# Kernel tuning notes

Hardware: AMD Instinct MI355X
Metric: run time of the kernel (lower is better)

Reference implementation:

```python
import jax, jax.numpy as jnp
import numpy as np

N, M, D, S = 4, 256, 32, 32


def setup_inputs() -> dict:
    key = jax.random.key(0)
    k1, k2 = jax.random.split(key)
    inputs = jax.random.normal(k1, (N, M, M, D), dtype=jnp.float32)
    mask = jnp.ones((N, M, 1), dtype=bool)
    coeffs = jax.random.normal(k2, (D, S, 15), dtype=jnp.float32) * np.sqrt(2.0) / (D + S)
    diag_bias = jnp.zeros((1, S, 1, 1), dtype=jnp.float32)
    all_bias = jnp.zeros((1, S, 1, 1), dtype=jnp.float32)
    return {"inputs": inputs, "mask": mask, "coeffs": coeffs,
            "diag_bias": diag_bias, "all_bias": all_bias}


def _contractions_2_to_2(x):
    # x: [N, D, m, m]; returns list of 15 [N, D, m, m] basis tensors ('inf' normalization)
    n, d, m, _ = x.shape
    diag = jnp.diagonal(x, axis1=2, axis2=3)            # [N, D, m]
    sum_diag = jnp.sum(diag, axis=2, keepdims=True)      # [N, D, 1]
    rows = jnp.sum(x, axis=3)                            # [N, D, m]
    cols = jnp.sum(x, axis=2)                            # [N, D, m]
    tot = jnp.sum(rows, axis=2)                          # [N, D]
    eye = jnp.eye(m, dtype=x.dtype)

    def diag_embed(v):  # v: [N, D, m] -> [N, D, m, m]
        return v[..., :, None] * eye

    full = x.shape
    op1 = diag_embed(diag)
    op2 = diag_embed(jnp.broadcast_to(sum_diag, diag.shape)) / m
    op3 = diag_embed(rows) / m
    op4 = diag_embed(cols) / m
    op5 = diag_embed(jnp.broadcast_to(tot[..., None], diag.shape)) / (m ** 2)
    op6 = jnp.broadcast_to(cols[..., :, None], full) / m
    op7 = jnp.broadcast_to(rows[..., :, None], full) / m
    op8 = jnp.broadcast_to(cols[..., None, :], full) / m
    op9 = jnp.broadcast_to(rows[..., None, :], full) / m
    op10 = x
    op11 = jnp.swapaxes(x, 2, 3)
    op12 = jnp.broadcast_to(diag[..., :, None], full)
    op13 = jnp.broadcast_to(diag[..., None, :], full)
    op14 = jnp.broadcast_to(sum_diag[..., None], full) / m
    op15 = jnp.broadcast_to(tot[..., None, None], full) / (m ** 2)
    return [op1, op2, op3, op4, op5, op6, op7, op8, op9, op10,
            op11, op12, op13, op14, op15]


def reference(inputs, mask, coeffs, diag_bias, all_bias):
    # inputs: [N, m, m, D] -> [N, D, m, m]
    x = jnp.transpose(inputs, (0, 3, 1, 2))
    m = x.shape[3]
    ops = _contractions_2_to_2(x)
    # einsum('dsb,ndbij->nsij') expressed as accumulation over the 15 bases
    # (avoids materializing the [N, D, 15, m, m] stack)
    out = jnp.zeros((x.shape[0], coeffs.shape[1], m, m), dtype=x.dtype)
    for b, op in enumerate(ops):
        out = out + jnp.einsum('ds,ndij->nsij', coeffs[:, :, b], op)
    eye = jnp.eye(m, dtype=x.dtype)[None, None]
    out = out + all_bias + eye * diag_bias
    return jnp.transpose(out, (0, 2, 3, 1))  # [N, m, m, S]
```

## Files before the change

### kernel.cpp

```cpp
#include <hip/hip_runtime.h>


#define NN 4
#define MM 256
#define DD 32
#define SS 32

#define WS_ROWS   0
#define WS_COLS   32768
#define WS_DIAG   65536
#define WS_RW     98304
#define WS_CW     131072
#define WS_DW     163840
#define WS_SD     196608
#define WS_TOT    196864
#define WS_C10    197120
#define WS_C11    198144

__global__ __launch_bounds__(256) void k_reduce(const float* __restrict__ in,
                                                float* __restrict__ ws) {
    float* rows = ws + WS_ROWS;
    float* cols = ws + WS_COLS;
    float* diagv = ws + WS_DIAG;
    int blk = blockIdx.x;
    bool do_cols = blk >= NN * MM;
    int nm = do_cols ? blk - NN * MM : blk;
    int n = nm >> 8;
    int ij = nm & 255;
    int t = threadIdx.x;
    int d = t & 31, g = t >> 5;
    float acc = 0.f;
    if (!do_cols) {
        const float* base = in + ((size_t)nm * MM) * DD + d;
        for (int j = g; j < MM; j += 8) acc += base[(size_t)j * DD];
    } else {
        const float* base = in + ((size_t)n * MM * MM + ij) * DD + d;
        for (int r = g; r < MM; r += 8) acc += base[(size_t)r * MM * DD];
    }
    __shared__ float red[256];
    red[t] = acc;
    __syncthreads();
    if (t < 32) {
        float s = 0.f;
        #pragma unroll
        for (int g2 = 0; g2 < 8; ++g2) s += red[g2 * 32 + t];
        if (!do_cols) {
            rows[nm * DD + t] = s;
            diagv[nm * DD + t] = in[(((size_t)nm) * MM + ij) * DD + t];
        } else {
            cols[nm * DD + t] = s;
        }
    }
}

__global__ __launch_bounds__(256) void k_small(const float* __restrict__ coeffs,
                                               float* __restrict__ ws) {
    if (blockIdx.x == 0) {
        int t = threadIdx.x;
        if (t < NN * DD) {
            int n = t >> 5, d = t & 31;
            const float* diagv = ws + WS_DIAG;
            const float* rows = ws + WS_ROWS;
            float s1 = 0.f, s2 = 0.f;
            for (int i = 0; i < MM; ++i) {
                s1 += diagv[(n * MM + i) * DD + d];
                s2 += rows[(n * MM + i) * DD + d];
            }
            ws[WS_SD + t] = s1;
            ws[WS_TOT + t] = s2;
        }
    } else {
        for (int idx = threadIdx.x; idx < DD * SS; idx += blockDim.x) {
            ws[WS_C10 + idx] = coeffs[idx * 15 + 9];
            ws[WS_C11 + idx] = coeffs[idx * 15 + 10];
        }
    }
}

__global__ __launch_bounds__(256) void k_aux(const float* __restrict__ coeffs,
                                             const float* __restrict__ diag_bias,
                                             const float* __restrict__ all_bias,
                                             float* __restrict__ ws) {
    int idx = blockIdx.x * blockDim.x + threadIdx.x;
    int s = idx & 31;
    int nm = idx >> 5;
    int n = nm >> 8;
    const float* rows = ws + WS_ROWS;
    const float* cols = ws + WS_COLS;
    const float* diagv = ws + WS_DIAG;
    const float inv_m = 1.0f / MM;
    const float inv_m2 = inv_m * inv_m;
    float u = 0.f, v = 0.f, dgacc = 0.f, w = 0.f;
    for (int d = 0; d < DD; ++d) {
        const float* c = coeffs + (d * SS + s) * 15;
        float r = rows[nm * DD + d];
        float cl = cols[nm * DD + d];
        float dv = diagv[nm * DD + d];
        float sdv = ws[WS_SD + n * DD + d];
        float totv = ws[WS_TOT + n * DD + d];
        u += c[5] * cl * inv_m + c[6] * r * inv_m + c[11] * dv;
        v += c[7] * cl * inv_m + c[8] * r * inv_m + c[12] * dv;
        dgacc += c[0] * dv + c[1] * sdv * inv_m + c[2] * r * inv_m
               + c[3] * cl * inv_m + c[4] * totv * inv_m2;
        w += c[13] * sdv * inv_m + c[14] * totv * inv_m2;
    }
    ws[WS_RW + idx] = u + w + all_bias[s];
    ws[WS_CW + idx] = v;
    ws[WS_DW + idx] = dgacc + diag_bias[s];
}

__global__ __launch_bounds__(256) void k_main(const float* __restrict__ in,
                                              const float* __restrict__ ws,
                                              float* __restrict__ out) {
    int b = blockIdx.x;
    int tjb = b & 15;
    int tib = (b >> 4) & 15;
    int n = b >> 8;
    int tj = threadIdx.x & 15, ti = threadIdx.x >> 4;
    int i = tib * 16 + ti, j = tjb * 16 + tj;

    const float* RW = ws + WS_RW;
    const float* CW = ws + WS_CW;
    const float* DW = ws + WS_DW;
    const float* c10 = ws + WS_C10;
    const float* c11 = ws + WS_C11;

    float acc[SS];
    {
        const float4* rw = (const float4*)(RW + (n * MM + i) * SS);
        const float4* cw = (const float4*)(CW + (n * MM + j) * SS);
        #pragma unroll
        for (int q = 0; q < 8; ++q) {
            float4 a = rw[q], bq = cw[q];
            acc[q * 4 + 0] = a.x + bq.x;
            acc[q * 4 + 1] = a.y + bq.y;
            acc[q * 4 + 2] = a.z + bq.z;
            acc[q * 4 + 3] = a.w + bq.w;
        }
        if (i == j) {
            const float4* dw = (const float4*)(DW + (n * MM + i) * SS);
            #pragma unroll
            for (int q = 0; q < 8; ++q) {
                float4 dq = dw[q];
                acc[q * 4 + 0] += dq.x;
                acc[q * 4 + 1] += dq.y;
                acc[q * 4 + 2] += dq.z;
                acc[q * 4 + 3] += dq.w;
            }
        }
    }

    const float4* A = (const float4*)(in + (((size_t)(n * MM + i)) * MM + j) * DD);
    const float4* B = (const float4*)(in + (((size_t)(n * MM + j)) * MM + i) * DD);
    #pragma unroll
    for (int dq = 0; dq < 8; ++dq) {
        float4 a4 = A[dq];
        float4 b4 = B[dq];
        const float* ca = c10 + dq * 4 * SS;
        const float* cb = c11 + dq * 4 * SS;
        #pragma unroll
        for (int r = 0; r < 4; ++r) {
            float av = (r == 0) ? a4.x : (r == 1) ? a4.y : (r == 2) ? a4.z : a4.w;
            float bv = (r == 0) ? b4.x : (r == 1) ? b4.y : (r == 2) ? b4.z : b4.w;
            #pragma unroll
            for (int s = 0; s < SS; ++s) {
                acc[s] = fmaf(av, ca[r * SS + s], acc[s]);
                acc[s] = fmaf(bv, cb[r * SS + s], acc[s]);
            }
        }
    }

    float4* o = (float4*)(out + (((size_t)(n * MM + i)) * MM + j) * SS);
    #pragma unroll
    for (int q = 0; q < 8; ++q) {
        o[q] = make_float4(acc[q * 4 + 0], acc[q * 4 + 1], acc[q * 4 + 2], acc[q * 4 + 3]);
    }
}

extern "C" void kernel_launch(void* const* d_in, const int* in_sizes, int n_in,
                              void* d_out, int out_size, void* d_ws, size_t ws_size,
                              hipStream_t stream) {
    const float* in = (const float*)d_in[0];
    const float* coeffs = (const float*)d_in[2];
    const float* diag_bias = (const float*)d_in[3];
    const float* all_bias = (const float*)d_in[4];
    float* out = (float*)d_out;
    float* ws = (float*)d_ws;

    k_reduce<<<2 * NN * MM, 256, 0, stream>>>(in, ws);
    k_small<<<2, 256, 0, stream>>>(coeffs, ws);
    k_aux<<<(NN * MM * SS) / 256, 256, 0, stream>>>(coeffs, diag_bias, all_bias, ws);
    k_main<<<NN * 16 * 16, 256, 0, stream>>>(in, ws, out);
}
```

Measured before the change: 179.7 us.

## Fuse small reductions into reduce kernel with atomics, repack coeffs, prefetch inputs

```diff
diff --git a/kernel.cpp b/kernel.cpp
--- a/kernel.cpp
+++ b/kernel.cpp
@@ -7,111 +7,96 @@
 #define SS 32
 
 #define WS_ROWS   0
-#define WS_COLS   32768
-#define WS_DIAG   65536
-#define WS_RW     98304
-#define WS_CW     131072
-#define WS_DW     163840
-#define WS_SD     196608
-#define WS_TOT    196864
-#define WS_C10    197120
-#define WS_C11    198144
+#define WS_COLSA  32768
+#define WS_COLSB  65536
+#define WS_DIAG   98304
+#define WS_RW     131072
+#define WS_CW     163840
+#define WS_DW     196608
+#define WS_SD     229376
+#define WS_TOT    229504
+#define WS_CPACK  229632
 
 __global__ __launch_bounds__(256) void k_reduce(const float* __restrict__ in,
+                                                const float* __restrict__ coeffs,
                                                 float* __restrict__ ws) {
-    float* rows = ws + WS_ROWS;
-    float* cols = ws + WS_COLS;
-    float* diagv = ws + WS_DIAG;
     int blk = blockIdx.x;
-    bool do_cols = blk >= NN * MM;
-    int nm = do_cols ? blk - NN * MM : blk;
-    int n = nm >> 8;
-    int ij = nm & 255;
     int t = threadIdx.x;
-    int d = t & 31, g = t >> 5;
-    float acc = 0.f;
-    if (!do_cols) {
-        const float* base = in + ((size_t)nm * MM) * DD + d;
+    if (blk < 256) {
+        int n = blk >> 6;
+        int rem = blk & 63;
+        int half = rem >> 5;
+        int jt = rem & 31;
+        int j = jt * 8 + (t >> 5);
+        int d = t & 31;
+        const float* base = in + ((size_t)n * MM * MM + j) * DD + d
+                               + (size_t)half * 128 * MM * DD;
+        float acc = 0.f;
+        #pragma unroll 8
+        for (int i = 0; i < 128; ++i) acc += base[(size_t)i * MM * DD];
+        float* dst = ws + (half ? WS_COLSB : WS_COLSA);
+        dst[(n * MM + j) * DD + d] = acc;
+    } else if (blk < 256 + NN * MM) {
+        int nm = blk - 256;
+        int n = nm >> 8;
+        int ii = nm & 255;
+        int d = t & 31, g = t >> 5;
+        const float* base = in + (size_t)nm * MM * DD + d;
+        float acc = 0.f;
         for (int j = g; j < MM; j += 8) acc += base[(size_t)j * DD];
+        __shared__ float red[256];
+        red[t] = acc;
+        __syncthreads();
+        if (t < 32) {
+            float s = 0.f;
+            #pragma unroll
+            for (int g2 = 0; g2 < 8; ++g2) s += red[g2 * 32 + t];
+            ws[WS_ROWS + nm * DD + t] = s;
+            float dv = in[((size_t)nm * MM + ii) * DD + t];
+            ws[WS_DIAG + nm * DD + t] = dv;
+            atomicAdd(ws + WS_TOT + n * DD + t, s);
+            atomicAdd(ws + WS_SD + n * DD + t, dv);
+        }
     } else {
-        const float* base = in + ((size_t)n * MM * MM + ij) * DD + d;
-        for (int r = g; r < MM; r += 8) acc += base[(size_t)r * MM * DD];
-    }
-    __shared__ float red[256];
-    red[t] = acc;
-    __syncthreads();
-    if (t < 32) {
-        float s = 0.f;
-        #pragma unroll
-        for (int g2 = 0; g2 < 8; ++g2) s += red[g2 * 32 + t];
-        if (!do_cols) {
-            rows[nm * DD + t] = s;
-            diagv[nm * DD + t] = in[(((size_t)nm) * MM + ij) * DD + t];
-        } else {
-            cols[nm * DD + t] = s;
+        for (int idx = t; idx < 15 * DD * SS; idx += 256) {
+            int plane = idx >> 10;
+            int ds = idx & 1023;
+            ws[WS_CPACK + plane * (DD * SS) + ds] = coeffs[ds * 15 + plane];
         }
     }
 }
 
-__global__ __launch_bounds__(256) void k_small(const float* __restrict__ coeffs,
-                                               float* __restrict__ ws) {
-    if (blockIdx.x == 0) {
-        int t = threadIdx.x;
-        if (t < NN * DD) {
-            int n = t >> 5, d = t & 31;
-            const float* diagv = ws + WS_DIAG;
-            const float* rows = ws + WS_ROWS;
-            float s1 = 0.f, s2 = 0.f;
-            for (int i = 0; i < MM; ++i) {
-                s1 += diagv[(n * MM + i) * DD + d];
-                s2 += rows[(n * MM + i) * DD + d];
-            }
-            ws[WS_SD + t] = s1;
-            ws[WS_TOT + t] = s2;
-        }
-    } else {
-        for (int idx = threadIdx.x; idx < DD * SS; idx += blockDim.x) {
-            ws[WS_C10 + idx] = coeffs[idx * 15 + 9];
-            ws[WS_C11 + idx] = coeffs[idx * 15 + 10];
-        }
-    }
-}
-
-__global__ __launch_bounds__(256) void k_aux(const float* __restrict__ coeffs,
-                                             const float* __restrict__ diag_bias,
+__global__ __launch_bounds__(256) void k_aux(const float* __restrict__ diag_bias,
                                              const float* __restrict__ all_bias,
                                              float* __restrict__ ws) {
     int idx = blockIdx.x * blockDim.x + threadIdx.x;
     int s = idx & 31;
     int nm = idx >> 5;
     int n = nm >> 8;
-    const float* rows = ws + WS_ROWS;
-    const float* cols = ws + WS_COLS;
-    const float* diagv = ws + WS_DIAG;
     const float inv_m = 1.0f / MM;
     const float inv_m2 = inv_m * inv_m;
     float u = 0.f, v = 0.f, dgacc = 0.f, w = 0.f;
     for (int d = 0; d < DD; ++d) {
-        const float* c = coeffs + (d * SS + s) * 15;
-        float r = rows[nm * DD + d];
-        float cl = cols[nm * DD + d];
-        float dv = diagv[nm * DD + d];
+        const float* cp = ws + WS_CPACK + d * SS + s;
+        float r = ws[WS_ROWS + nm * DD + d];
+        float cl = ws[WS_COLSA + nm * DD + d] + ws[WS_COLSB + nm * DD + d];
+        float dv = ws[WS_DIAG + nm * DD + d];
         float sdv = ws[WS_SD + n * DD + d];
         float totv = ws[WS_TOT + n * DD + d];
-        u += c[5] * cl * inv_m + c[6] * r * inv_m + c[11] * dv;
-        v += c[7] * cl * inv_m + c[8] * r * inv_m + c[12] * dv;
-        dgacc += c[0] * dv + c[1] * sdv * inv_m + c[2] * r * inv_m
-               + c[3] * cl * inv_m + c[4] * totv * inv_m2;
-        w += c[13] * sdv * inv_m + c[14] * totv * inv_m2;
+        u += cp[5 * 1024] * cl * inv_m + cp[6 * 1024] * r * inv_m + cp[11 * 1024] * dv;
+        v += cp[7 * 1024] * cl * inv_m + cp[8 * 1024] * r * inv_m + cp[12 * 1024] * dv;
+        dgacc += cp[0] * dv + cp[1 * 1024] * sdv * inv_m + cp[2 * 1024] * r * inv_m
+               + cp[3 * 1024] * cl * inv_m + cp[4 * 1024] * totv * inv_m2;
+        w += cp[13 * 1024] * sdv * inv_m + cp[14 * 1024] * totv * inv_m2;
     }
     ws[WS_RW + idx] = u + w + all_bias[s];
     ws[WS_CW + idx] = v;
     ws[WS_DW + idx] = dgacc + diag_bias[s];
 }
 
-__global__ __launch_bounds__(256) void k_main(const float* __restrict__ in,
-                                              const float* __restrict__ ws,
-                                              float* __restrict__ out) {
+__global__ __launch_bounds__(256, 2) void k_main(const float* __restrict__ in,
+                                                 const float* __restrict__ ws,
+                                                 float* __restrict__ out) {
     int b = blockIdx.x;
     int tjb = b & 15;
     int tib = (b >> 4) & 15;
@@ -119,62 +104,60 @@
     int tj = threadIdx.x & 15, ti = threadIdx.x >> 4;
     int i = tib * 16 + ti, j = tjb * 16 + tj;
 
-    const float* RW = ws + WS_RW;
-    const float* CW = ws + WS_CW;
-    const float* DW = ws + WS_DW;
-    const float* c10 = ws + WS_C10;
-    const float* c11 = ws + WS_C11;
+    const float4* A = (const float4*)(in + (((size_t)(n * MM + i)) * MM + j) * DD);
+    const float4* B = (const float4*)(in + (((size_t)(n * MM + j)) * MM + i) * DD);
 
+    float4 av[8], bv[8];
+    #pragma unroll
+    for (int q = 0; q < 8; ++q) av[q] = A[q];
+    #pragma unroll
+    for (int q = 0; q < 8; ++q) bv[q] = B[q];
+
+    const float4* rw = (const float4*)(ws + WS_RW + (n * MM + i) * SS);
+    const float4* cw = (const float4*)(ws + WS_CW + (n * MM + j) * SS);
     float acc[SS];
-    {
-        const float4* rw = (const float4*)(RW + (n * MM + i) * SS);
-        const float4* cw = (const float4*)(CW + (n * MM + j) * SS);
+    #pragma unroll
+    for (int q = 0; q < 8; ++q) {
+        float4 x = rw[q], y = cw[q];
+        acc[q * 4 + 0] = x.x + y.x;
+        acc[q * 4 + 1] = x.y + y.y;
+        acc[q * 4 + 2] = x.z + y.z;
+        acc[q * 4 + 3] = x.w + y.w;
+    }
+    if (i == j) {
+        const float4* dw = (const float4*)(ws + WS_DW + (n * MM + i) * SS);
         #pragma unroll
         for (int q = 0; q < 8; ++q) {
-            float4 a = rw[q], bq = cw[q];
-            acc[q * 4 + 0] = a.x + bq.x;
-            acc[q * 4 + 1] = a.y + bq.y;
-            acc[q * 4 + 2] = a.z + bq.z;
-            acc[q * 4 + 3] = a.w + bq.w;
-        }
-        if (i == j) {
-            const float4* dw = (const float4*)(DW + (n * MM + i) * SS);
-            #pragma unroll
-            for (int q = 0; q < 8; ++q) {
-                float4 dq = dw[q];
-                acc[q * 4 + 0] += dq.x;
-                acc[q * 4 + 1] += dq.y;
-                acc[q * 4 + 2] += dq.z;
-                acc[q * 4 + 3] += dq.w;
-            }
+            float4 dq = dw[q];
+            acc[q * 4 + 0] += dq.x;
+            acc[q * 4 + 1] += dq.y;
+            acc[q * 4 + 2] += dq.z;
+            acc[q * 4 + 3] += dq.w;
         }
     }
 
-    const float4* A = (const float4*)(in + (((size_t)(n * MM + i)) * MM + j) * DD);
-    const float4* B = (const float4*)(in + (((size_t)(n * MM + j)) * MM + i) * DD);
+    const float* c10 = ws + WS_CPACK + 9 * (DD * SS);
+    const float* c11 = ws + WS_CPACK + 10 * (DD * SS);
     #pragma unroll
     for (int dq = 0; dq < 8; ++dq) {
-        float4 a4 = A[dq];
-        float4 b4 = B[dq];
         const float* ca = c10 + dq * 4 * SS;
         const float* cb = c11 + dq * 4 * SS;
         #pragma unroll
         for (int r = 0; r < 4; ++r) {
-            float av = (r == 0) ? a4.x : (r == 1) ? a4.y : (r == 2) ? a4.z : a4.w;
-            float bv = (r == 0) ? b4.x : (r == 1) ? b4.y : (r == 2) ? b4.z : b4.w;
+            float a = (r == 0) ? av[dq].x : (r == 1) ? av[dq].y : (r == 2) ? av[dq].z : av[dq].w;
+            float bb = (r == 0) ? bv[dq].x : (r == 1) ? bv[dq].y : (r == 2) ? bv[dq].z : bv[dq].w;
             #pragma unroll
             for (int s = 0; s < SS; ++s) {
-                acc[s] = fmaf(av, ca[r * SS + s], acc[s]);
-                acc[s] = fmaf(bv, cb[r * SS + s], acc[s]);
+                acc[s] = fmaf(a, ca[r * SS + s], acc[s]);
+                acc[s] = fmaf(bb, cb[r * SS + s], acc[s]);
             }
         }
     }
 
     float4* o = (float4*)(out + (((size_t)(n * MM + i)) * MM + j) * SS);
     #pragma unroll
-    for (int q = 0; q < 8; ++q) {
+    for (int q = 0; q < 8; ++q)
         o[q] = make_float4(acc[q * 4 + 0], acc[q * 4 + 1], acc[q * 4 + 2], acc[q * 4 + 3]);
-    }
 }
 
 extern "C" void kernel_launch(void* const* d_in, const int* in_sizes, int n_in,
@@ -187,8 +170,8 @@
     float* out = (float*)d_out;
     float* ws = (float*)d_ws;
 
-    k_reduce<<<2 * NN * MM, 256, 0, stream>>>(in, ws);
-    k_small<<<2, 256, 0, stream>>>(coeffs, ws);
-    k_aux<<<(NN * MM * SS) / 256, 256, 0, stream>>>(coeffs, diag_bias, all_bias, ws);
+    hipMemsetAsync((char*)d_ws + (size_t)WS_SD * 4, 0, 256 * sizeof(float), stream);
+    k_reduce<<<256 + NN * MM + 1, 256, 0, stream>>>(in, coeffs, ws);
+    k_aux<<<(NN * MM * SS) / 256, 256, 0, stream>>>(diag_bias, all_bias, ws);
     k_main<<<NN * 16 * 16, 256, 0, stream>>>(in, ws, out);
 }
```

Result: faster. 146.7 us (-18.4%).
